# Performance work log

Measured on AMD Instinct MI355X. Metric: run time of the kernel, lower is better.

The kernel has to match this reference:

```python
import jax, jax.numpy as jnp
import numpy as np

MAX_REL = 64  # max_relative_position
LN_EPS = 1e-5


def _relative_positions(seq_len):
    r = jnp.arange(seq_len)
    rel = jnp.clip(r[None, :] - r[:, None], -MAX_REL, MAX_REL) + MAX_REL
    return rel  # [S, S] int32 in [0, 2*MAX_REL]


def setup_inputs() -> dict:
    key = jax.random.key(0)
    ks = jax.random.split(key, 8)
    B, S, H = 8, 1024, 128
    sd = 1.0 / np.sqrt(H)
    return {
        "x": jax.random.normal(ks[0], (B, S, H), jnp.float32),
        "Wq": jax.random.normal(ks[1], (H, H), jnp.float32) * sd,
        "bq": jnp.zeros((H,), jnp.float32),
        "Wk": jax.random.normal(ks[2], (H, H), jnp.float32) * sd,
        "bk": jnp.zeros((H,), jnp.float32),
        "Wv": jax.random.normal(ks[3], (H, H), jnp.float32) * sd,
        "bv": jnp.zeros((H,), jnp.float32),
        "rel_k": jax.random.normal(ks[4], (2 * MAX_REL + 1, H), jnp.float32),
        "rel_v": jax.random.normal(ks[5], (2 * MAX_REL + 1, H), jnp.float32),
        "Wo": jax.random.normal(ks[6], (H, H), jnp.float32) * sd,
        "bo": jnp.zeros((H,), jnp.float32),
        "gamma": jnp.ones((H,), jnp.float32),
        "beta": jnpp if False else jnp.zeros((H,), jnp.float32),
    }


def reference(x, Wq, bq, Wk, bk, Wv, bv, rel_k, rel_v, Wo, bo, gamma, beta):
    B, S, H = x.shape
    scale = jnp.sqrt(jnp.asarray(H, x.dtype))

    q = x @ Wq + bq  # [B,S,H]
    k = x @ Wk + bk
    v = x @ Wv + bv

    scores = jnp.einsum("bih,bjh->bij", q, k) / scale  # [B,S,S]

    relpos = _relative_positions(S)            # [S,S] int
    rk = rel_k[relpos]                          # [S,S,H] gather
    scores = scores + jnp.einsum("bih,ijh->bij", q, rk)

    attn = jax.nn.softmax(scores, axis=-1)      # dropout = identity (eval)

    ctx = jnp.einsum("bij,bjh->bih", attn, v)
    rv = rel_v[relpos]                          # [S,S,H] gather
    ctx = ctx + jnp.einsum("bij,ijh->bih", attn, rv)

    out = ctx @ Wo + bo

    # residual + LayerNorm
    y = out + x
    mu = jnp.mean(y, axis=-1, keepdims=True)
    var = jnp.mean(jnp.square(y - mu), axis=-1, keepdims=True)
    y = (y - mu) * jax.lax.rsqrt(var + LN_EPS) * gamma + beta
    return y, attn
```

## Files before the change

kernel.cpp:

```cpp
#include <hip/hip_runtime.h>

constexpr int Bn = 8, Sn = 1024, Hn = 128, Rn = 129, RLD = 132;
constexpr float INV_SCALE = 0.088388347648318447f;
constexpr size_t YEL = (size_t)Bn * Sn * Hn;

typedef short bf16x8 __attribute__((ext_vector_type(8)));
typedef short v4s __attribute__((ext_vector_type(4)));
typedef float f32x4 __attribute__((ext_vector_type(4)));
typedef int v4i __attribute__((ext_vector_type(4)));

__device__ __forceinline__ float bf2f(short s) {
    unsigned u = ((unsigned)(unsigned short)s) << 16;
    float f; __builtin_memcpy(&f, &u, 4); return f;
}
__device__ __forceinline__ short f2bf(float f) {
    unsigned u; __builtin_memcpy(&u, &f, 4);
    unsigned r = (u + 0x7fffu + ((u >> 16) & 1u)) >> 16;
    return (short)(r & 0xffffu);
}

__global__ __launch_bounds__(384) void build_relcat(
    const float* __restrict__ rel_k, short* __restrict__ relcat)
{
    const int p = blockIdx.x, c = threadIdx.x;
    const int j = (c < 256) ? (c & 127) : (c - 256);
    float v = rel_k[p * Hn + j];
    short h = f2bf(v);
    relcat[p * 384 + c] = (c < 256) ? h : f2bf(v - bf2f(h));
}

__global__ __launch_bounds__(256) void build_bcat(
    const float* __restrict__ rel_v, const float* __restrict__ Wo,
    short* __restrict__ BcatT)
{
    int idx = blockIdx.x * 256 + threadIdx.x;
    int k = idx >> 7, n = idx & 127;
    float v;
    if (k < 128) v = Wo[k * Hn + n];
    else if (k < 257) {
        int p = k - 128; float a = 0.f;
        for (int h = 0; h < Hn; ++h) a += rel_v[p * Hn + h] * Wo[h * Hn + n];
        v = a;
    } else v = 0.f;
    BcatT[n * 320 + k] = f2bf(v);
}

__global__ __launch_bounds__(256) void proj(
    const float* __restrict__ X,
    const float* __restrict__ Wq, const float* __restrict__ bq,
    const float* __restrict__ Wk, const float* __restrict__ bk,
    const float* __restrict__ Wv, const float* __restrict__ bv,
    short* __restrict__ qh, short* __restrict__ qcat,
    short* __restrict__ kh, short* __restrict__ vT)
{
    __shared__ float xs[64][128];
    __shared__ float wsm[32][128];
    const int tid = threadIdx.x;
    const int sel = blockIdx.y;
    const int row0 = blockIdx.x * 64;
    const float* W = (sel == 0) ? Wq : (sel == 1) ? Wk : Wv;
    const float* bias = (sel == 0) ? bq : (sel == 1) ? bk : bv;

#pragma unroll
    for (int it = 0; it < 8; ++it) {
        int u = tid + it * 256;
        int r = u >> 5, c4 = (u & 31) * 4;
        *(float4*)&xs[r][c4] = *(const float4*)(X + (size_t)(row0 + r) * 128 + c4);
    }

    const int rg = tid >> 5, cg = tid & 31;
    float acc[8][4] = {};
    for (int kc = 0; kc < 128; kc += 32) {
#pragma unroll
        for (int it = 0; it < 4; ++it) {
            int u = tid + it * 256;
            int kk = u >> 5, c4 = (u & 31) * 4;
            *(float4*)&wsm[kk][c4] = *(const float4*)(W + (size_t)(kc + kk) * 128 + c4);
        }
        __syncthreads();
#pragma unroll 8
        for (int kk = 0; kk < 32; ++kk) {
            float wv[4];
#pragma unroll
            for (int c = 0; c < 4; ++c) wv[c] = wsm[kk][cg + c * 32];
#pragma unroll
            for (int r = 0; r < 8; ++r) {
                float xv = xs[rg * 8 + r][kc + kk];
#pragma unroll
                for (int c = 0; c < 4; ++c) acc[r][c] += xv * wv[c];
            }
        }
        __syncthreads();
    }

#pragma unroll
    for (int c = 0; c < 4; ++c) {
        int col = cg + c * 32;
        float bv2 = bias[col];
#pragma unroll
        for (int r = 0; r < 8; ++r) {
            int row = row0 + rg * 8 + r;
            float v = acc[r][c] + bv2;
            short h = f2bf(v);
            if (sel == 0) {
                qh[(size_t)row * 128 + col] = h;
                qcat[(size_t)row * 256 + col] = h;
                qcat[(size_t)row * 256 + 128 + col] = f2bf(v - bf2f(h));
            } else if (sel == 1) {
                kh[(size_t)row * 128 + col] = h;
            } else {
                int b = row >> 10, i = row & (Sn - 1);
                vT[(size_t)b * 131072 + (size_t)col * 1024 + i] = h;
            }
        }
    }
}

__global__ __launch_bounds__(256) void qrel_gemm(
    const short* __restrict__ qcat, const short* __restrict__ relcat,
    float* __restrict__ qrel)
{
    __shared__ short As[64][72];
    __shared__ short Bs[64][72];
    const int tid = threadIdx.x;
    const int wave = tid >> 6, lane = tid & 63;
    const int quad = lane >> 4, l15 = lane & 15;
    const int row0 = blockIdx.x * 64, col0 = blockIdx.y * 64;

    f32x4 acc[4] = {};
    for (int kc = 0; kc < 384; kc += 64) {
#pragma unroll
        for (int it = 0; it < 2; ++it) {
            int u = tid + it * 256;
            int r = u >> 3, c8 = (u & 7) * 8;
            int srcc = kc + c8;
            if (srcc >= 256) srcc -= 256;
            *(v4i*)&As[r][c8] = *(const v4i*)(qcat + (size_t)(row0 + r) * 256 + srcc);
        }
#pragma unroll
        for (int it = 0; it < 2; ++it) {
            int u = tid + it * 256;
            int r = u >> 3, c8 = (u & 7) * 8;
            v4i val = {0, 0, 0, 0};
            if (col0 + r < Rn)
                val = *(const v4i*)(relcat + (size_t)(col0 + r) * 384 + kc + c8);
            *(v4i*)&Bs[r][c8] = val;
        }
        __syncthreads();
#pragma unroll
        for (int ks = 0; ks < 64; ks += 32) {
            bf16x8 af = *(const bf16x8*)&As[wave * 16 + l15][ks + quad * 8];
#pragma unroll
            for (int nt = 0; nt < 4; ++nt) {
                bf16x8 bf = *(const bf16x8*)&Bs[nt * 16 + l15][ks + quad * 8];
                acc[nt] = __builtin_amdgcn_mfma_f32_16x16x32_bf16(af, bf, acc[nt], 0, 0, 0);
            }
        }
        __syncthreads();
    }
    const int rloc0 = wave * 16 + quad * 4;
#pragma unroll
    for (int nt = 0; nt < 4; ++nt) {
        int col = col0 + nt * 16 + l15;
#pragma unroll
        for (int r = 0; r < 4; ++r) {
            if (col < Rn)
                qrel[(size_t)(row0 + rloc0 + r) * RLD + col] = acc[nt][r];
        }
    }
}

__global__ __launch_bounds__(512, 4) void fused_attn(
    const short* __restrict__ qh, const short* __restrict__ kh,
    const short* __restrict__ vT, const float* __restrict__ qrel_g,
    float* __restrict__ attn_g, float* __restrict__ arel_g,
    float* __restrict__ ctx_g)
{
    __shared__ __align__(16) short Pb[16][1048];
    __shared__ float QrL[16][132];
    __shared__ float redM[16][8], redS[16][8], redL[16][8], redH[16][8];

    const int tid = threadIdx.x;
    const int w = tid >> 6, lane = tid & 63;
    const int quad = lane >> 4, l15 = lane & 15;
    const int bz = blockIdx.z;
    const int row0 = blockIdx.x * 16;
    const size_t grow0 = (size_t)bz * Sn + row0;

#pragma unroll
    for (int rr = 0; rr < 2; ++rr) {
        int r = w * 2 + rr;
        const float* src = qrel_g + (grow0 + r) * RLD;
        QrL[r][lane] = src[lane];
        QrL[r][lane + 64] = src[lane + 64];
        if (lane < 4) QrL[r][128 + lane] = src[128 + lane];
    }

    bf16x8 afr[4];
#pragma unroll
    for (int kk = 0; kk < 4; ++kk)
        afr[kk] = *(const bf16x8*)(qh + (grow0 + l15) * 128 + kk * 32 + quad * 8);

    const short* khb = kh + (size_t)bz * Sn * 128;
    f32x4 acc[8] = {};
    bf16x8 bb[2][4];
#pragma unroll
    for (int kk = 0; kk < 4; ++kk)
        bb[0][kk] = *(const bf16x8*)(khb + (size_t)(w * 128 + l15) * 128 + kk * 32 + quad * 8);
#pragma unroll
    for (int nt = 0; nt < 8; ++nt) {
        int cur = nt & 1;
        if (nt < 7) {
#pragma unroll
            for (int kk = 0; kk < 4; ++kk)
                bb[cur ^ 1][kk] = *(const bf16x8*)(khb +
                    (size_t)(w * 128 + (nt + 1) * 16 + l15) * 128 + kk * 32 + quad * 8);
        }
#pragma unroll
        for (int kk = 0; kk < 4; ++kk)
            acc[nt] = __builtin_amdgcn_mfma_f32_16x16x32_bf16(afr[kk], bb[cur][kk], acc[nt], 0, 0, 0);
    }
    __syncthreads();

    float mx[4];
#pragma unroll
    for (int r = 0; r < 4; ++r) {
        int lr = quad * 4 + r, i = row0 + lr;
        float m = -3.4e38f;
#pragma unroll
        for (int nt = 0; nt < 8; ++nt) {
            int col = w * 128 + nt * 16 + l15;
            int d = col - i; d = (d < -64) ? -64 : (d > 64 ? 64 : d);
            float v = acc[nt][r] * INV_SCALE + QrL[lr][d + 64];
            acc[nt][r] = v;
            m = fmaxf(m, v);
        }
#pragma unroll
        for (int msk = 1; msk < 16; msk <<= 1) m = fmaxf(m, __shfl_xor(m, msk));
        if (l15 == 0) redM[lr][w] = m;
    }
    __syncthreads();
#pragma unroll
    for (int r = 0; r < 4; ++r) {
        int lr = quad * 4 + r;
        float m = redM[lr][0];
#pragma unroll
        for (int j = 1; j < 8; ++j) m = fmaxf(m, redM[lr][j]);
        mx[r] = m;
    }

#pragma unroll
    for (int r = 0; r < 4; ++r) {
        int lr = quad * 4 + r, i = row0 + lr;
        float s = 0.f, lo = 0.f, hi = 0.f;
#pragma unroll
        for (int nt = 0; nt < 8; ++nt) {
            float e = __expf(acc[nt][r] - mx[r]);
            acc[nt][r] = e;
            s += e;
            int col = w * 128 + nt * 16 + l15;
            lo += (col <= i - 64) ? e : 0.f;
            hi += (col >= i + 64) ? e : 0.f;
        }
#pragma unroll
        for (int msk = 1; msk < 16; msk <<= 1) {
            s += __shfl_xor(s, msk);
            lo += __shfl_xor(lo, msk);
            hi += __shfl_xor(hi, msk);
        }
        if (l15 == 0) { redS[lr][w] = s; redL[lr][w] = lo; redH[lr][w] = hi; }
    }
    __syncthreads();

#pragma unroll
    for (int r = 0; r < 4; ++r) {
        int lr = quad * 4 + r;
        float s = 0.f;
#pragma unroll
        for (int j = 0; j < 8; ++j) s += redS[lr][j];
        float inv = 1.0f / s;
        float* arow = attn_g + (grow0 + lr) * Sn;
#pragma unroll
        for (int nt = 0; nt < 8; ++nt) {
            int col = w * 128 + nt * 16 + l15;
            float v = acc[nt][r] * inv;
            arow[col] = v;
            Pb[lr][col] = f2bf(v);
        }
    }
    __syncthreads();

#pragma unroll
    for (int rr = 0; rr < 2; ++rr) {
        int lr = w * 2 + rr, i = row0 + lr;
        float s = 0.f, lo = 0.f, hi = 0.f;
#pragma unroll
        for (int j = 0; j < 8; ++j) { s += redS[lr][j]; lo += redL[lr][j]; hi += redH[lr][j]; }
        float inv = 1.0f / s;
        float* arow = arel_g + (grow0 + lr) * RLD;
        float v0;
        if (lane == 0) v0 = lo * inv;
        else { int c = i + lane - 64; v0 = (c >= 0 && c < Sn) ? bf2f(Pb[lr][c]) : 0.f; }
        arow[lane] = v0;
        int c1 = i + lane;
        arow[lane + 64] = (c1 < Sn) ? bf2f(Pb[lr][c1]) : 0.f;
        if (lane < 4) arow[128 + lane] = (lane == 0) ? hi * inv : 0.f;
    }

    f32x4 cacc = {};
    const short* vtb = vT + (size_t)bz * 131072 + (size_t)(w * 16 + l15) * 1024;
#pragma unroll 8
    for (int kk = 0; kk < 32; ++kk) {
        bf16x8 a = *(const bf16x8*)&Pb[l15][kk * 32 + quad * 8];
        bf16x8 b = *(const bf16x8*)(vtb + kk * 32 + quad * 8);
        cacc = __builtin_amdgcn_mfma_f32_16x16x32_bf16(a, b, cacc, 0, 0, 0);
    }
#pragma unroll
    for (int r = 0; r < 4; ++r)
        ctx_g[(grow0 + quad * 4 + r) * 128 + w * 16 + l15] = cacc[r];
}

__global__ __launch_bounds__(256, 4) void ln_gemm(
    const float* __restrict__ ctx, const float* __restrict__ arel,
    const short* __restrict__ BcatT, const float* __restrict__ bo,
    const float* __restrict__ X, const float* __restrict__ gamma,
    const float* __restrict__ beta, float* __restrict__ y)
{
    __shared__ float rs1[16][4];
    __shared__ float rs2[16][4];
    const int tid = threadIdx.x;
    const int w = tid >> 6, lane = tid & 63;
    const int quad = lane >> 4, l15 = lane & 15;
    const int rows0 = blockIdx.x * 16;
    const int arow = rows0 + l15;

    f32x4 acc[2] = {};
#pragma unroll
    for (int kk = 0; kk < 9; ++kk) {
        bf16x8 a;
        if (kk < 4) {
            const float* src = ctx + (size_t)arow * 128 + kk * 32 + quad * 8;
            float4 w0 = *(const float4*)src, w1 = *(const float4*)(src + 4);
            short t[8] = { f2bf(w0.x), f2bf(w0.y), f2bf(w0.z), f2bf(w0.w),
                           f2bf(w1.x), f2bf(w1.y), f2bf(w1.z), f2bf(w1.w) };
            __builtin_memcpy(&a, t, 16);
        } else if (kk < 8) {
            const float* src = arel + (size_t)arow * RLD + (kk - 4) * 32 + quad * 8;
            float4 w0 = *(const float4*)src, w1 = *(const float4*)(src + 4);
            short t[8] = { f2bf(w0.x), f2bf(w0.y), f2bf(w0.z), f2bf(w0.w),
                           f2bf(w1.x), f2bf(w1.y), f2bf(w1.z), f2bf(w1.w) };
            __builtin_memcpy(&a, t, 16);
        } else {
            short t[8] = {0,0,0,0,0,0,0,0};
            if (quad == 0) {
                float4 w0 = *(const float4*)(arel + (size_t)arow * RLD + 128);
                t[0] = f2bf(w0.x); t[1] = f2bf(w0.y); t[2] = f2bf(w0.z); t[3] = f2bf(w0.w);
            }
            __builtin_memcpy(&a, t, 16);
        }
#pragma unroll
        for (int t2 = 0; t2 < 2; ++t2) {
            int n = (w * 2 + t2) * 16 + l15;
            bf16x8 b = *(const bf16x8*)(BcatT + (size_t)n * 320 + kk * 32 + quad * 8);
            acc[t2] = __builtin_amdgcn_mfma_f32_16x16x32_bf16(a, b, acc[t2], 0, 0, 0);
        }
    }

    float vv[2][4];
#pragma unroll
    for (int t2 = 0; t2 < 2; ++t2) {
        int col = w * 32 + t2 * 16 + l15;
        float bv = bo[col];
#pragma unroll
        for (int r = 0; r < 4; ++r) {
            int grow = rows0 + quad * 4 + r;
            vv[t2][r] = acc[t2][r] + bv + X[(size_t)grow * 128 + col];
        }
    }
#pragma unroll
    for (int r = 0; r < 4; ++r) {
        float s = vv[0][r] + vv[1][r];
#pragma unroll
        for (int m = 1; m < 16; m <<= 1) s += __shfl_xor(s, m);
        if (l15 == 0) rs1[quad * 4 + r][w] = s;
    }
    __syncthreads();
    float mu[4];
#pragma unroll
    for (int r = 0; r < 4; ++r) {
        int lr = quad * 4 + r;
        mu[r] = (rs1[lr][0] + rs1[lr][1] + rs1[lr][2] + rs1[lr][3]) * (1.f / 128.f);
    }
#pragma unroll
    for (int r = 0; r < 4; ++r) {
        float d0 = vv[0][r] - mu[r], d1 = vv[1][r] - mu[r];
        float s = d0 * d0 + d1 * d1;
#pragma unroll
        for (int m = 1; m < 16; m <<= 1) s += __shfl_xor(s, m);
        if (l15 == 0) rs2[quad * 4 + r][w] = s;
    }
    __syncthreads();
#pragma unroll
    for (int r = 0; r < 4; ++r) {
        int lr = quad * 4 + r;
        int grow = rows0 + lr;
        float var = (rs2[lr][0] + rs2[lr][1] + rs2[lr][2] + rs2[lr][3]) * (1.f / 128.f);
        float inv = rsqrtf(var + 1e-5f);
#pragma unroll
        for (int t2 = 0; t2 < 2; ++t2) {
            int col = w * 32 + t2 * 16 + l15;
            y[(size_t)grow * 128 + col] = (vv[t2][r] - mu[r]) * inv * gamma[col] + beta[col];
        }
    }
}

extern "C" void kernel_launch(void* const* d_in, const int* in_sizes, int n_in,
                              void* d_out, int out_size, void* d_ws, size_t ws_size,
                              hipStream_t stream) {
    const float* x     = (const float*)d_in[0];
    const float* Wq    = (const float*)d_in[1];
    const float* bq    = (const float*)d_in[2];
    const float* Wk    = (const float*)d_in[3];
    const float* bk    = (const float*)d_in[4];
    const float* Wv    = (const float*)d_in[5];
    const float* bv    = (const float*)d_in[6];
    const float* rel_k = (const float*)d_in[7];
    const float* rel_v = (const float*)d_in[8];
    const float* Wo    = (const float*)d_in[9];
    const float* bo    = (const float*)d_in[10];
    const float* gamma = (const float*)d_in[11];
    const float* beta  = (const float*)d_in[12];

    char* ws = (char*)d_ws;
    short* qh     = (short*)(ws + 0);
    short* kh     = (short*)(ws + 2097152);
    short* vT     = (short*)(ws + 4194304);
    short* qcat   = (short*)(ws + 6291456);
    float* qrel   = (float*)(ws + 10485760);
    short* relcat = (short*)(ws + 14811136);
    short* BcatT  = (short*)relcat;
    float* ctx    = (float*)qcat;

    float* y_out = (float*)d_out;
    float* attn  = (float*)d_out + YEL;

    build_relcat<<<dim3(Rn), 384, 0, stream>>>(rel_k, relcat);
    proj<<<dim3(128, 3), 256, 0, stream>>>(x, Wq, bq, Wk, bk, Wv, bv, qh, qcat, kh, vT);
    qrel_gemm<<<dim3(128, 3), 256, 0, stream>>>(qcat, relcat, qrel);
    build_bcat<<<dim3(160), 256, 0, stream>>>(rel_v, Wo, BcatT);

    fused_attn<<<dim3(64, 1, Bn), 512, 0, stream>>>(qh, kh, vT, qrel, attn, qrel, ctx);

    ln_gemm<<<dim3(512), 256, 0, stream>>>(ctx, qrel, BcatT, bo, x, gamma, beta, y_out);
}
```

Baseline: 172.5 us.

## Fuse output projection and LayerNorm into attention kernel with LDS-staged K/V tiles

Folds the former ln_gemm kernel (output projection with concatenated rel_v/Wo weights, residual add, LayerNorm) into the end of fused_attn. The context and relative-attention buckets are now kept in shared memory as bf16 instead of going through global memory. K and V^T tiles are staged cooperatively into LDS, 128 keys at a time, rather than each wave loading its own slice directly from global, and the column-to-wave mapping changes to match. This removes one kernel launch and a global round trip of the intermediates. In exchange it uses about 80 KB of LDS per block, which limits occupancy, and adds many __syncthreads barriers.

```diff
diff --git a/kernel.cpp b/kernel.cpp
--- a/kernel.cpp
+++ b/kernel.cpp
@@ -173,12 +173,20 @@
 __global__ __launch_bounds__(512, 4) void fused_attn(
     const short* __restrict__ qh, const short* __restrict__ kh,
     const short* __restrict__ vT, const float* __restrict__ qrel_g,
-    float* __restrict__ attn_g, float* __restrict__ arel_g,
-    float* __restrict__ ctx_g)
+    const short* __restrict__ BcatT,
+    const float* __restrict__ X, const float* __restrict__ bo,
+    const float* __restrict__ gamma, const float* __restrict__ beta,
+    float* __restrict__ attn_g, float* __restrict__ y_g)
 {
-    __shared__ __align__(16) short Pb[16][1048];
-    __shared__ float QrL[16][132];
-    __shared__ float redM[16][8], redS[16][8], redL[16][8], redH[16][8];
+    __shared__ __align__(16) char smem[80896];
+    short* KTs  = (short*)smem;
+    short* Pb   = (short*)(smem + 34816);
+    short* CtxA = (short*)(smem + 67840);
+    float* QrL  = (float*)(smem + 67840);
+    float* redM = (float*)(smem + 78848);
+    float* redS = redM + 128;
+    float* redL = redS + 128;
+    float* redH = redL + 128;
 
     const int tid = threadIdx.x;
     const int w = tid >> 6, lane = tid & 63;
@@ -191,9 +199,9 @@
     for (int rr = 0; rr < 2; ++rr) {
         int r = w * 2 + rr;
         const float* src = qrel_g + (grow0 + r) * RLD;
-        QrL[r][lane] = src[lane];
-        QrL[r][lane + 64] = src[lane + 64];
-        if (lane < 4) QrL[r][128 + lane] = src[128 + lane];
+        QrL[r * 132 + lane] = src[lane];
+        QrL[r * 132 + 64 + lane] = src[64 + lane];
+        if (lane < 4) QrL[r * 132 + 128 + lane] = src[128 + lane];
     }
 
     bf16x8 afr[4];
@@ -203,24 +211,21 @@
 
     const short* khb = kh + (size_t)bz * Sn * 128;
     f32x4 acc[8] = {};
-    bf16x8 bb[2][4];
-#pragma unroll
-    for (int kk = 0; kk < 4; ++kk)
-        bb[0][kk] = *(const bf16x8*)(khb + (size_t)(w * 128 + l15) * 128 + kk * 32 + quad * 8);
-#pragma unroll
-    for (int nt = 0; nt < 8; ++nt) {
-        int cur = nt & 1;
-        if (nt < 7) {
-#pragma unroll
-            for (int kk = 0; kk < 4; ++kk)
-                bb[cur ^ 1][kk] = *(const bf16x8*)(khb +
-                    (size_t)(w * 128 + (nt + 1) * 16 + l15) * 128 + kk * 32 + quad * 8);
-        }
-#pragma unroll
-        for (int kk = 0; kk < 4; ++kk)
-            acc[nt] = __builtin_amdgcn_mfma_f32_16x16x32_bf16(afr[kk], bb[cur][kk], acc[nt], 0, 0, 0);
-    }
-    __syncthreads();
+    for (int kt = 0; kt < 8; ++kt) {
+#pragma unroll
+        for (int it = 0; it < 4; ++it) {
+            int u = tid + it * 512;
+            int r = u >> 4, c8 = (u & 15) * 8;
+            *(v4i*)&KTs[r * 136 + c8] = *(const v4i*)(khb + (size_t)(kt * 128 + r) * 128 + c8);
+        }
+        __syncthreads();
+#pragma unroll
+        for (int kk = 0; kk < 4; ++kk) {
+            bf16x8 b = *(const bf16x8*)&KTs[(w * 16 + l15) * 136 + kk * 32 + quad * 8];
+            acc[kt] = __builtin_amdgcn_mfma_f32_16x16x32_bf16(afr[kk], b, acc[kt], 0, 0, 0);
+        }
+        __syncthreads();
+    }
 
     float mx[4];
 #pragma unroll
@@ -228,24 +233,24 @@
         int lr = quad * 4 + r, i = row0 + lr;
         float m = -3.4e38f;
 #pragma unroll
-        for (int nt = 0; nt < 8; ++nt) {
-            int col = w * 128 + nt * 16 + l15;
+        for (int kt = 0; kt < 8; ++kt) {
+            int col = kt * 128 + w * 16 + l15;
             int d = col - i; d = (d < -64) ? -64 : (d > 64 ? 64 : d);
-            float v = acc[nt][r] * INV_SCALE + QrL[lr][d + 64];
-            acc[nt][r] = v;
+            float v = acc[kt][r] * INV_SCALE + QrL[lr * 132 + d + 64];
+            acc[kt][r] = v;
             m = fmaxf(m, v);
         }
 #pragma unroll
         for (int msk = 1; msk < 16; msk <<= 1) m = fmaxf(m, __shfl_xor(m, msk));
-        if (l15 == 0) redM[lr][w] = m;
+        if (l15 == 0) redM[lr * 8 + w] = m;
     }
     __syncthreads();
 #pragma unroll
     for (int r = 0; r < 4; ++r) {
         int lr = quad * 4 + r;
-        float m = redM[lr][0];
-#pragma unroll
-        for (int j = 1; j < 8; ++j) m = fmaxf(m, redM[lr][j]);
+        float m = redM[lr * 8];
+#pragma unroll
+        for (int j = 1; j < 8; ++j) m = fmaxf(m, redM[lr * 8 + j]);
         mx[r] = m;
     }
 
@@ -254,11 +259,11 @@
         int lr = quad * 4 + r, i = row0 + lr;
         float s = 0.f, lo = 0.f, hi = 0.f;
 #pragma unroll
-        for (int nt = 0; nt < 8; ++nt) {
-            float e = __expf(acc[nt][r] - mx[r]);
-            acc[nt][r] = e;
+        for (int kt = 0; kt < 8; ++kt) {
+            float e = __expf(acc[kt][r] - mx[r]);
+            acc[kt][r] = e;
             s += e;
-            int col = w * 128 + nt * 16 + l15;
+            int col = kt * 128 + w * 16 + l15;
             lo += (col <= i - 64) ? e : 0.f;
             hi += (col >= i + 64) ? e : 0.f;
         }
@@ -268,7 +273,7 @@
             lo += __shfl_xor(lo, msk);
             hi += __shfl_xor(hi, msk);
         }
-        if (l15 == 0) { redS[lr][w] = s; redL[lr][w] = lo; redH[lr][w] = hi; }
+        if (l15 == 0) { redS[lr * 8 + w] = s; redL[lr * 8 + w] = lo; redH[lr * 8 + w] = hi; }
     }
     __syncthreads();
 
@@ -277,140 +282,130 @@
         int lr = quad * 4 + r;
         float s = 0.f;
 #pragma unroll
-        for (int j = 0; j < 8; ++j) s += redS[lr][j];
+        for (int j = 0; j < 8; ++j) s += redS[lr * 8 + j];
         float inv = 1.0f / s;
         float* arow = attn_g + (grow0 + lr) * Sn;
 #pragma unroll
-        for (int nt = 0; nt < 8; ++nt) {
-            int col = w * 128 + nt * 16 + l15;
-            float v = acc[nt][r] * inv;
+        for (int kt = 0; kt < 8; ++kt) {
+            int col = kt * 128 + w * 16 + l15;
+            float v = acc[kt][r] * inv;
             arow[col] = v;
-            Pb[lr][col] = f2bf(v);
-        }
-    }
-    __syncthreads();
-
+            Pb[lr * 1032 + col] = f2bf(v);
+        }
+    }
+    __syncthreads();
+
+    const short* vtb = vT + (size_t)bz * 131072;
+    f32x4 cacc = {};
+    for (int kc = 0; kc < 8; ++kc) {
+#pragma unroll
+        for (int it = 0; it < 4; ++it) {
+            int u = tid + it * 512;
+            int r = u >> 4, c8 = (u & 15) * 8;
+            *(v4i*)&KTs[r * 136 + c8] = *(const v4i*)(vtb + (size_t)r * 1024 + kc * 128 + c8);
+        }
+        __syncthreads();
+#pragma unroll
+        for (int kk = 0; kk < 4; ++kk) {
+            bf16x8 a = *(const bf16x8*)&Pb[l15 * 1032 + kc * 128 + kk * 32 + quad * 8];
+            bf16x8 b = *(const bf16x8*)&KTs[(w * 16 + l15) * 136 + kk * 32 + quad * 8];
+            cacc = __builtin_amdgcn_mfma_f32_16x16x32_bf16(a, b, cacc, 0, 0, 0);
+        }
+        __syncthreads();
+    }
+
+#pragma unroll
+    for (int r = 0; r < 4; ++r)
+        CtxA[(quad * 4 + r) * 344 + w * 16 + l15] = f2bf(cacc[r]);
 #pragma unroll
     for (int rr = 0; rr < 2; ++rr) {
         int lr = w * 2 + rr, i = row0 + lr;
         float s = 0.f, lo = 0.f, hi = 0.f;
 #pragma unroll
-        for (int j = 0; j < 8; ++j) { s += redS[lr][j]; lo += redL[lr][j]; hi += redH[lr][j]; }
+        for (int j = 0; j < 8; ++j) {
+            s += redS[lr * 8 + j]; lo += redL[lr * 8 + j]; hi += redH[lr * 8 + j];
+        }
         float inv = 1.0f / s;
-        float* arow = arel_g + (grow0 + lr) * RLD;
         float v0;
         if (lane == 0) v0 = lo * inv;
-        else { int c = i + lane - 64; v0 = (c >= 0 && c < Sn) ? bf2f(Pb[lr][c]) : 0.f; }
-        arow[lane] = v0;
+        else { int c = i + lane - 64; v0 = (c >= 0 && c < Sn) ? bf2f(Pb[lr * 1032 + c]) : 0.f; }
+        CtxA[lr * 344 + 128 + lane] = f2bf(v0);
         int c1 = i + lane;
-        arow[lane + 64] = (c1 < Sn) ? bf2f(Pb[lr][c1]) : 0.f;
-        if (lane < 4) arow[128 + lane] = (lane == 0) ? hi * inv : 0.f;
-    }
-
-    f32x4 cacc = {};
-    const short* vtb = vT + (size_t)bz * 131072 + (size_t)(w * 16 + l15) * 1024;
-#pragma unroll 8
-    for (int kk = 0; kk < 32; ++kk) {
-        bf16x8 a = *(const bf16x8*)&Pb[l15][kk * 32 + quad * 8];
-        bf16x8 b = *(const bf16x8*)(vtb + kk * 32 + quad * 8);
-        cacc = __builtin_amdgcn_mfma_f32_16x16x32_bf16(a, b, cacc, 0, 0, 0);
-    }
-#pragma unroll
-    for (int r = 0; r < 4; ++r)
-        ctx_g[(grow0 + quad * 4 + r) * 128 + w * 16 + l15] = cacc[r];
-}
-
-__global__ __launch_bounds__(256, 4) void ln_gemm(
-    const float* __restrict__ ctx, const float* __restrict__ arel,
-    const short* __restrict__ BcatT, const float* __restrict__ bo,
-    const float* __restrict__ X, const float* __restrict__ gamma,
-    const float* __restrict__ beta, float* __restrict__ y)
-{
-    __shared__ float rs1[16][4];
-    __shared__ float rs2[16][4];
-    const int tid = threadIdx.x;
-    const int w = tid >> 6, lane = tid & 63;
-    const int quad = lane >> 4, l15 = lane & 15;
-    const int rows0 = blockIdx.x * 16;
-    const int arow = rows0 + l15;
-
-    f32x4 acc[2] = {};
-#pragma unroll
-    for (int kk = 0; kk < 9; ++kk) {
-        bf16x8 a;
-        if (kk < 4) {
-            const float* src = ctx + (size_t)arow * 128 + kk * 32 + quad * 8;
-            float4 w0 = *(const float4*)src, w1 = *(const float4*)(src + 4);
-            short t[8] = { f2bf(w0.x), f2bf(w0.y), f2bf(w0.z), f2bf(w0.w),
-                           f2bf(w1.x), f2bf(w1.y), f2bf(w1.z), f2bf(w1.w) };
-            __builtin_memcpy(&a, t, 16);
-        } else if (kk < 8) {
-            const float* src = arel + (size_t)arow * RLD + (kk - 4) * 32 + quad * 8;
-            float4 w0 = *(const float4*)src, w1 = *(const float4*)(src + 4);
-            short t[8] = { f2bf(w0.x), f2bf(w0.y), f2bf(w0.z), f2bf(w0.w),
-                           f2bf(w1.x), f2bf(w1.y), f2bf(w1.z), f2bf(w1.w) };
-            __builtin_memcpy(&a, t, 16);
+        CtxA[lr * 344 + 192 + lane] = (c1 < Sn) ? Pb[lr * 1032 + c1] : (short)0;
+        CtxA[lr * 344 + 256 + lane] = (lane == 0) ? f2bf(hi * inv) : (short)0;
+    }
+    __syncthreads();
+
+    f32x4 yacc = {};
+#pragma unroll
+    for (int ch = 0; ch < 3; ++ch) {
+        if (ch < 2) {
+#pragma unroll
+            for (int it = 0; it < 4; ++it) {
+                int u = tid + it * 512;
+                int n = u >> 4, c8 = (u & 15) * 8;
+                *(v4i*)&KTs[n * 136 + c8] = *(const v4i*)(BcatT + (size_t)n * 320 + ch * 128 + c8);
+            }
         } else {
-            short t[8] = {0,0,0,0,0,0,0,0};
-            if (quad == 0) {
-                float4 w0 = *(const float4*)(arel + (size_t)arow * RLD + 128);
-                t[0] = f2bf(w0.x); t[1] = f2bf(w0.y); t[2] = f2bf(w0.z); t[3] = f2bf(w0.w);
+#pragma unroll
+            for (int it = 0; it < 2; ++it) {
+                int u = tid + it * 512;
+                int n = u >> 3, c8 = (u & 7) * 8;
+                *(v4i*)&KTs[n * 136 + c8] = *(const v4i*)(BcatT + (size_t)n * 320 + 256 + c8);
             }
-            __builtin_memcpy(&a, t, 16);
-        }
-#pragma unroll
-        for (int t2 = 0; t2 < 2; ++t2) {
-            int n = (w * 2 + t2) * 16 + l15;
-            bf16x8 b = *(const bf16x8*)(BcatT + (size_t)n * 320 + kk * 32 + quad * 8);
-            acc[t2] = __builtin_amdgcn_mfma_f32_16x16x32_bf16(a, b, acc[t2], 0, 0, 0);
-        }
-    }
-
-    float vv[2][4];
-#pragma unroll
-    for (int t2 = 0; t2 < 2; ++t2) {
-        int col = w * 32 + t2 * 16 + l15;
-        float bv = bo[col];
-#pragma unroll
-        for (int r = 0; r < 4; ++r) {
-            int grow = rows0 + quad * 4 + r;
-            vv[t2][r] = acc[t2][r] + bv + X[(size_t)grow * 128 + col];
-        }
-    }
-#pragma unroll
-    for (int r = 0; r < 4; ++r) {
-        float s = vv[0][r] + vv[1][r];
-#pragma unroll
-        for (int m = 1; m < 16; m <<= 1) s += __shfl_xor(s, m);
-        if (l15 == 0) rs1[quad * 4 + r][w] = s;
+        }
+        __syncthreads();
+        const int nkk = (ch == 2) ? 2 : 4;
+        for (int kk = 0; kk < nkk; ++kk) {
+            bf16x8 a = *(const bf16x8*)&CtxA[l15 * 344 + ch * 128 + kk * 32 + quad * 8];
+            bf16x8 b = *(const bf16x8*)&KTs[(w * 16 + l15) * 136 + kk * 32 + quad * 8];
+            yacc = __builtin_amdgcn_mfma_f32_16x16x32_bf16(a, b, yacc, 0, 0, 0);
+        }
+        __syncthreads();
+    }
+
+    const int col = w * 16 + l15;
+    const float bov = bo[col], gv = gamma[col], bev = beta[col];
+    float vv[4];
+#pragma unroll
+    for (int r = 0; r < 4; ++r) {
+        int lr = quad * 4 + r;
+        vv[r] = yacc[r] + bov + X[(grow0 + lr) * 128 + col];
+    }
+#pragma unroll
+    for (int r = 0; r < 4; ++r) {
+        float s = vv[r];
+#pragma unroll
+        for (int msk = 1; msk < 16; msk <<= 1) s += __shfl_xor(s, msk);
+        if (l15 == 0) redM[(quad * 4 + r) * 8 + w] = s;
     }
     __syncthreads();
     float mu[4];
 #pragma unroll
     for (int r = 0; r < 4; ++r) {
         int lr = quad * 4 + r;
-        mu[r] = (rs1[lr][0] + rs1[lr][1] + rs1[lr][2] + rs1[lr][3]) * (1.f / 128.f);
-    }
-#pragma unroll
-    for (int r = 0; r < 4; ++r) {
-        float d0 = vv[0][r] - mu[r], d1 = vv[1][r] - mu[r];
-        float s = d0 * d0 + d1 * d1;
-#pragma unroll
-        for (int m = 1; m < 16; m <<= 1) s += __shfl_xor(s, m);
-        if (l15 == 0) rs2[quad * 4 + r][w] = s;
+        float s = 0.f;
+#pragma unroll
+        for (int j = 0; j < 8; ++j) s += redM[lr * 8 + j];
+        mu[r] = s * (1.f / 128.f);
+    }
+#pragma unroll
+    for (int r = 0; r < 4; ++r) {
+        float d = vv[r] - mu[r];
+        float s = d * d;
+#pragma unroll
+        for (int msk = 1; msk < 16; msk <<= 1) s += __shfl_xor(s, msk);
+        if (l15 == 0) redS[(quad * 4 + r) * 8 + w] = s;
     }
     __syncthreads();
 #pragma unroll
     for (int r = 0; r < 4; ++r) {
         int lr = quad * 4 + r;
-        int grow = rows0 + lr;
-        float var = (rs2[lr][0] + rs2[lr][1] + rs2[lr][2] + rs2[lr][3]) * (1.f / 128.f);
-        float inv = rsqrtf(var + 1e-5f);
-#pragma unroll
-        for (int t2 = 0; t2 < 2; ++t2) {
-            int col = w * 32 + t2 * 16 + l15;
-            y[(size_t)grow * 128 + col] = (vv[t2][r] - mu[r]) * inv * gamma[col] + beta[col];
-        }
+        float s = 0.f;
+#pragma unroll
+        for (int j = 0; j < 8; ++j) s += redS[lr * 8 + j];
+        float inv = rsqrtf(s * (1.f / 128.f) + 1e-5f);
+        y_g[(grow0 + lr) * 128 + col] = (vv[r] - mu[r]) * inv * gv + bev;
     }
 }
 
@@ -439,7 +434,6 @@
     float* qrel   = (float*)(ws + 10485760);
     short* relcat = (short*)(ws + 14811136);
     short* BcatT  = (short*)relcat;
-    float* ctx    = (float*)qcat;
 
     float* y_out = (float*)d_out;
     float* attn  = (float*)d_out + YEL;
@@ -449,7 +443,6 @@
     qrel_gemm<<<dim3(128, 3), 256, 0, stream>>>(qcat, relcat, qrel);
     build_bcat<<<dim3(160), 256, 0, stream>>>(rel_v, Wo, BcatT);
 
-    fused_attn<<<dim3(64, 1, Bn), 512, 0, stream>>>(qh, kh, vT, qrel, attn, qrel, ctx);
-
-    ln_gemm<<<dim3(512), 256, 0, stream>>>(ctx, qrel, BcatT, bo, x, gamma, beta, y_out);
-}
+    fused_attn<<<dim3(64, 1, Bn), 512, 0, stream>>>(
+        qh, kh, vT, qrel, BcatT, x, bo, gamma, beta, attn, y_out);
+}
```

After: 160.4 us. 1.08x faster.
